# Kernel tuning notes

Measured on AMD Instinct MI355X. Metric: run time of the kernel, lower is better.

Reference implementation:

```python
import jax, jax.numpy as jnp
import numpy as np

N_NODES = 50000
N_EDGES = 800000
HID = 128
EDGE_FEAT = 4
NUM_G = 20
R_MIN, R_MAX = 0.0, 100.0  # r_max = 10.0**2


def _mlp2(x, w1, b1, w2, b2, act_last):
    y = jax.nn.relu(x @ w1 + b1)
    y = y @ w2 + b2
    return jax.nn.relu(y) if act_last else y


def _linear_init(key, fan_in, fan_out):
    kw, kb = jax.random.split(key)
    lim = 1.0 / np.sqrt(fan_in)
    w = jax.random.uniform(kw, (fan_in, fan_out), jnp.float32, -lim, lim)
    b = jax.random.uniform(kb, (fan_out,), jnp.float32, -lim, lim)
    return w, b


def setup_inputs():
    key = jax.random.key(0)
    ks = jax.random.split(key, 16)
    src = jax.random.randint(ks[0], (N_EDGES,), 0, N_NODES)
    dst = jax.random.randint(ks[1], (N_EDGES,), 0, N_NODES)
    edge_feat = jax.random.normal(ks[2], (N_EDGES, EDGE_FEAT), jnp.float32)
    h = jax.random.normal(ks[3], (N_NODES, HID), jnp.float32)
    x = jax.random.normal(ks[4], (N_NODES, 3), jnp.float32)
    ein = 2 * HID + EDGE_FEAT + NUM_G
    ew1, eb1 = _linear_init(ks[5], ein, HID)
    ew2, eb2 = _linear_init(ks[6], HID, HID)
    infw, infb = _linear_init(ks[7], HID, 1)
    xw1, xb1 = _linear_init(ks[8], HID, HID)
    xw2, xb2 = _linear_init(ks[9], HID, 1)
    nw1, nb1 = _linear_init(ks[10], 2 * HID, HID)
    nw2, nb2 = _linear_init(ks[11], HID, HID)
    return {"src": src, "dst": dst, "edge_feat": edge_feat, "h": h, "x": x,
            "ew1": ew1, "eb1": eb1, "ew2": ew2, "eb2": eb2,
            "infw": infw, "infb": infb,
            "xw1": xw1, "xb1": xb1, "xw2": xw2, "xb2": xb2,
            "nw1": nw1, "nb1": nb1, "nw2": nw2, "nb2": nb2}


def reference(src, dst, edge_feat, h, x,
              ew1, eb1, ew2, eb2, infw, infb,
              xw1, xb1, xw2, xb2, nw1, nb1, nw2, nb2):
    n_nodes = h.shape[0]
    rel_x = x[dst] - x[src]                      # [E, 3]
    r = jnp.sum(rel_x * rel_x, -1, keepdims=True)  # [E, 1]
    # GaussianSmearing expansion
    offsets = jnp.linspace(R_MIN, R_MAX, NUM_G)
    coeff = -0.5 / (offsets[1] - offsets[0]) ** 2
    r_feat = jnp.exp(coeff * (r - offsets) ** 2)  # [E, NUM_G]
    # edge message MLP (act_last=True)
    cat = jnp.concatenate([edge_feat, r_feat, h[dst], h[src]], axis=-1)
    mij = _mlp2(cat, ew1, eb1, ew2, eb2, act_last=True)  # [E, HID]
    eij = jax.nn.sigmoid(mij @ infw + infb)              # [E, 1]
    mi = jax.ops.segment_sum(mij * eij, dst, num_segments=n_nodes)  # [N, HID]
    h_new = h + _mlp2(jnp.concatenate([mi, h], -1), nw1, nb1, nw2, nb2, act_last=False)
    # coordinate update: (xi - xj) == rel_x
    x_scale = _mlp2(mij, xw1, xb1, xw2, xb2, act_last=False)  # [E, 1]
    delta_x = jax.ops.segment_sum(rel_x * x_scale, dst, num_segments=n_nodes)
    x_new = x + delta_x
    return h_new, x_new
```

## Files before the change

kernel.cpp:

```cpp
#include <hip/hip_runtime.h>

#define HID 128
#define NNODES 50000
#define NEDGES 800000

typedef __attribute__((ext_vector_type(8))) short short8;
typedef __attribute__((ext_vector_type(4))) float f32x4;

union U8 { short8 v; unsigned short u[8]; };

__device__ __forceinline__ unsigned short f2b(float f) {
  unsigned int u = __float_as_uint(f);
  u += 0x7FFFu + ((u >> 16) & 1u);
  return (unsigned short)(u >> 16);
}

__device__ __forceinline__ unsigned int pk2(float a, float b) {
  unsigned int ua = __float_as_uint(a);
  ua += 0x7FFFu + ((ua >> 16) & 1u);
  unsigned int ub = __float_as_uint(b);
  ub += 0x7FFFu + ((ub >> 16) & 1u);
  return (ua >> 16) | (ub & 0xFFFF0000u);
}

__device__ __forceinline__ unsigned int pk2h(float a, float b) {
  unsigned int ua = __float_as_uint(a) + 0x8000u;
  unsigned int ub = __float_as_uint(b) + 0x8000u;
  return (ua >> 16) | (ub & 0xFFFF0000u);
}

__device__ __forceinline__ void atomicPkAddBf16(unsigned short* addr, unsigned int packed) {
  asm volatile("global_atomic_pk_add_bf16 %0, %1, off" :: "v"(addr), "v"(packed) : "memory");
}

__device__ __forceinline__ int stage_chunk(int c0, int row) {
  return ((c0 >> 3) ^ (row & 7) ^ (((row >> 2) & 3) << 1)) & 15;
}

__global__ __launch_bounds__(256) void pack_kernel(
    const float* __restrict__ ew1, const float* __restrict__ ew2,
    const float* __restrict__ xw1, const float* __restrict__ nw1,
    const float* __restrict__ nw2, unsigned short* __restrict__ ws) {
  int i = blockIdx.x * 256 + threadIdx.x;
  const float* w; int base, ksrc;
  if (i < 36864)       { w = ew1; base = 0;      ksrc = 280; }
  else if (i < 53248)  { w = ew2; base = 36864;  ksrc = 128; }
  else if (i < 69632)  { w = xw1; base = 53248;  ksrc = 128; }
  else if (i < 102400) { w = nw1; base = 69632;  ksrc = 256; }
  else if (i < 118784) { w = nw2; base = 102400; ksrc = 128; }
  else return;
  int li = i - base;
  int j = li & 7, t = li >> 3;
  int col = t & 127, kg = t >> 7;
  int k = kg * 8 + j;
  float v = (k < ksrc) ? w[k * 128 + col] : 0.0f;
  ws[i] = f2b(v);
}

__global__ __launch_bounds__(256) void hpack_kernel(
    const float* __restrict__ h, unsigned short* __restrict__ hB) {
  int i = blockIdx.x * 256 + threadIdx.x;
  const float4* p = reinterpret_cast<const float4*>(h + (size_t)i * 8);
  float4 a = p[0], b = p[1];
  uint4 u;
  u.x = pk2(a.x, a.y); u.y = pk2(a.z, a.w);
  u.z = pk2(b.x, b.y); u.w = pk2(b.z, b.w);
  *reinterpret_cast<uint4*>(hB + (size_t)i * 8) = u;
}

template<int MODE>
__global__ __launch_bounds__(512, 8) void edge_kernel(
    const int* __restrict__ src, const int* __restrict__ dst,
    const float* __restrict__ ef, const float* __restrict__ h,
    const float* __restrict__ x,
    const float* __restrict__ eb1, const float* __restrict__ eb2,
    const float* __restrict__ infw, const float* __restrict__ infb,
    const float* __restrict__ xb1, const float* __restrict__ xw2,
    const float* __restrict__ xb2,
    const short8* __restrict__ W1p, const short8* __restrict__ W2p,
    const short8* __restrict__ XW1p,
    const unsigned short* __restrict__ hB,
    float* __restrict__ miF, unsigned short* __restrict__ miB,
    float* __restrict__ dx) {
  __shared__ __align__(16) char catB[64 * 576];
  __shared__ int dL[64], sL[64];
  __shared__ float relL[64][3];
  __shared__ float ppart[8][64];
  __shared__ float eijL[64];

  const int tid = threadIdx.x;
  const int e0 = blockIdx.x * 64;
  const int lane = tid & 63, w = tid >> 6;
  const int wm = w >> 2, wn = w & 3;
  const int lr = lane & 15, lg = lane >> 4;
  const int l7 = lr & 7, l3 = lr & 3;
  const int colb = wn*32 + lr;
  const int c00 = wn*32 + lg*4, c01 = c00 + 16;
  const int rbase = wm*32;

  {
    int row = tid >> 3, sub = tid & 7;
    int e = e0 + row;
    int s = src[e], d = dst[e];
    if (sub == 0) { sL[row] = s; dL[row] = d; }
    float rx = x[3*d+0] - x[3*s+0];
    float ry = x[3*d+1] - x[3*s+1];
    float rz = x[3*d+2] - x[3*s+2];
    if (sub == 1) { relL[row][0] = rx; relL[row][1] = ry; relL[row][2] = rz; }
    float r = rx*rx + ry*ry + rz*rz;
    const float step = 100.0f / 19.0f;
    const float co = -0.5f / (step * step);
    if (sub < 6) {
      float v4[4];
      if (sub == 0) {
        const float4 efv = reinterpret_cast<const float4*>(ef)[e];
        v4[0]=efv.x; v4[1]=efv.y; v4[2]=efv.z; v4[3]=efv.w;
      } else {
        #pragma unroll
        for (int q = 0; q < 4; ++q) {
          float g = (float)(sub*4 - 4 + q) * step;
          float t = r - g;
          v4[q] = __expf(co * t * t);
        }
      }
      int c = sub*4;
      int chunk = (c>>3) ^ (row&7);
      uint2 pv; pv.x = pk2h(v4[0], v4[1]); pv.y = pk2h(v4[2], v4[3]);
      *reinterpret_cast<uint2*>(catB + row*576 + (chunk<<4) + ((c&7)<<1)) = pv;
    } else if (sub == 6) {
      U8 z;
      #pragma unroll
      for (int j = 0; j < 8; ++j) z.u[j] = 0;
      *reinterpret_cast<short8*>(catB + row*576 + ((32 + (3 ^ (row&3)))<<4)) = z.v;
    }
  }

  #pragma unroll
  for (int it = 0; it < 4; ++it) {
    int i = tid + it*512;
    int row = i >> 5, c = i & 31;
    int node = (c < 16) ? dst[e0+row] : src[e0+row];
    int chunk = 3 + c;
    int sw = (chunk < 32) ? (chunk ^ (row&7)) : (32 + ((chunk&3) ^ (row&3)));
    if (MODE == 2) {
      short8 u = *reinterpret_cast<const short8*>(hB + (size_t)node*128 + (c&15)*8);
      *reinterpret_cast<short8*>(catB + row*576 + (sw<<4)) = u;
    } else {
      const float4* hp = reinterpret_cast<const float4*>(h + (size_t)node*128 + (c&15)*8);
      float4 a = hp[0], b = hp[1];
      uint4 u;
      u.x = pk2(a.x, a.y); u.y = pk2(a.z, a.w);
      u.z = pk2(b.x, b.y); u.w = pk2(b.z, b.w);
      *reinterpret_cast<uint4*>(catB + row*576 + (sw<<4)) = u;
    }
  }

  short8 p00 = W1p[(0*4+lg)*128 + colb], p01 = W1p[(0*4+lg)*128 + colb + 16];
  short8 p10 = W1p[(1*4+lg)*128 + colb], p11 = W1p[(1*4+lg)*128 + colb + 16];
  __syncthreads();

  f32x4 acc[2][2];
  #pragma unroll
  for (int t = 0; t < 2; ++t) { acc[t][0] = (f32x4)0.0f; acc[t][1] = (f32x4)0.0f; }
  #pragma unroll
  for (int kt = 0; kt < 9; ++kt) {
    int ch = (kt < 8) ? ((kt*4+lg) ^ l7) : (32 + (lg ^ l3));
    short8 a0 = *reinterpret_cast<const short8*>(catB + (rbase + 0*16 + lr)*576 + (ch<<4));
    short8 a1 = *reinterpret_cast<const short8*>(catB + (rbase + 1*16 + lr)*576 + (ch<<4));
    short8 b0, b1;
    if (kt == 0)      { b0 = p00; b1 = p01; }
    else if (kt == 1) { b0 = p10; b1 = p11; }
    else              { b0 = W1p[(kt*4+lg)*128 + colb]; b1 = W1p[(kt*4+lg)*128 + colb + 16]; }
    acc[0][0] = __builtin_amdgcn_mfma_f32_16x16x32_bf16(b0, a0, acc[0][0], 0, 0, 0);
    acc[0][1] = __builtin_amdgcn_mfma_f32_16x16x32_bf16(b1, a0, acc[0][1], 0, 0, 0);
    acc[1][0] = __builtin_amdgcn_mfma_f32_16x16x32_bf16(b0, a1, acc[1][0], 0, 0, 0);
    acc[1][1] = __builtin_amdgcn_mfma_f32_16x16x32_bf16(b1, a1, acc[1][1], 0, 0, 0);
  }
  __syncthreads();

  {
    float4 be0 = *reinterpret_cast<const float4*>(eb1 + c00);
    float4 be1 = *reinterpret_cast<const float4*>(eb1 + c01);
    #pragma unroll
    for (int t = 0; t < 2; ++t) {
      int row = rbase + t*16 + lr;
      char* rowB = catB + row*576;
      #pragma unroll
      for (int j = 0; j < 2; ++j) {
        const float4 be = j ? be1 : be0;
        int c0 = j ? c01 : c00;
        float v0 = fmaxf(acc[t][j][0] + be.x, 0.f);
        float v1 = fmaxf(acc[t][j][1] + be.y, 0.f);
        float v2 = fmaxf(acc[t][j][2] + be.z, 0.f);
        float v3 = fmaxf(acc[t][j][3] + be.w, 0.f);
        uint2 pv; pv.x = pk2h(v0, v1); pv.y = pk2h(v2, v3);
        int chunk = (c0>>3) ^ (row&7);
        *reinterpret_cast<uint2*>(rowB + (chunk<<4) + ((c0&7)<<1)) = pv;
      }
    }
  }
  __syncthreads();

  f32x4 acc2[2][2];
  #pragma unroll
  for (int t = 0; t < 2; ++t) { acc2[t][0] = (f32x4)0.0f; acc2[t][1] = (f32x4)0.0f; }
  #pragma unroll
  for (int kt = 0; kt < 4; ++kt) {
    int ch = (kt*4+lg) ^ l7;
    short8 a0 = *reinterpret_cast<const short8*>(catB + (rbase + 0*16 + lr)*576 + (ch<<4));
    short8 a1 = *reinterpret_cast<const short8*>(catB + (rbase + 1*16 + lr)*576 + (ch<<4));
    short8 b0 = W2p[(kt*4+lg)*128 + colb];
    short8 b1 = W2p[(kt*4+lg)*128 + colb + 16];
    acc2[0][0] = __builtin_amdgcn_mfma_f32_16x16x32_bf16(b0, a0, acc2[0][0], 0, 0, 0);
    acc2[0][1] = __builtin_amdgcn_mfma_f32_16x16x32_bf16(b1, a0, acc2[0][1], 0, 0, 0);
    acc2[1][0] = __builtin_amdgcn_mfma_f32_16x16x32_bf16(b0, a1, acc2[1][0], 0, 0, 0);
    acc2[1][1] = __builtin_amdgcn_mfma_f32_16x16x32_bf16(b1, a1, acc2[1][1], 0, 0, 0);
  }
  {
    float4 be0 = *reinterpret_cast<const float4*>(eb2 + c00);
    float4 be1 = *reinterpret_cast<const float4*>(eb2 + c01);
    float4 iw0 = *reinterpret_cast<const float4*>(infw + c00);
    float4 iw1 = *reinterpret_cast<const float4*>(infw + c01);
    float pl[2];
    #pragma unroll
    for (int t = 0; t < 2; ++t) {
      int row = rbase + t*16 + lr;
      char* rowB = catB + row*576;
      pl[t] = 0.f;
      #pragma unroll
      for (int j = 0; j < 2; ++j) {
        const float4 be = j ? be1 : be0;
        const float4 iw = j ? iw1 : iw0;
        int c0 = j ? c01 : c00;
        float v0 = fmaxf(acc2[t][j][0] + be.x, 0.f);
        float v1 = fmaxf(acc2[t][j][1] + be.y, 0.f);
        float v2 = fmaxf(acc2[t][j][2] + be.z, 0.f);
        float v3 = fmaxf(acc2[t][j][3] + be.w, 0.f);
        acc2[t][j][0]=v0; acc2[t][j][1]=v1; acc2[t][j][2]=v2; acc2[t][j][3]=v3;
        pl[t] += v0*iw.x + v1*iw.y + v2*iw.z + v3*iw.w;
        uint2 pv; pv.x = pk2h(v0, v1); pv.y = pk2h(v2, v3);
        int chunk = 16 + ((c0>>3) ^ (row&7));
        *reinterpret_cast<uint2*>(rowB + (chunk<<4) + ((c0&7)<<1)) = pv;
      }
    }
    #pragma unroll
    for (int t = 0; t < 2; ++t) {
      pl[t] += __shfl_xor(pl[t], 16, 64);
      pl[t] += __shfl_xor(pl[t], 32, 64);
    }
    if (lane < 16) {
      #pragma unroll
      for (int t = 0; t < 2; ++t) ppart[w][rbase + t*16 + lane] = pl[t];
    }
  }
  __syncthreads();

  if (tid < 64) {
    int wmr = tid >> 5;
    float s2 = infb[0] + ppart[wmr*4+0][tid] + ppart[wmr*4+1][tid]
                       + ppart[wmr*4+2][tid] + ppart[wmr*4+3][tid];
    eijL[tid] = 1.f / (1.f + __expf(-s2));
  }
  __syncthreads();

  if (MODE >= 1) {
    #pragma unroll
    for (int t = 0; t < 2; ++t) {
      int row = rbase + t*16 + lr;
      float e = eijL[row];
      char* rowB = catB + row*576;
      #pragma unroll
      for (int j = 0; j < 2; ++j) {
        int c0 = j ? c01 : c00;
        uint2 pv;
        pv.x = pk2h(acc2[t][j][0]*e, acc2[t][j][1]*e);
        pv.y = pk2h(acc2[t][j][2]*e, acc2[t][j][3]*e);
        *reinterpret_cast<uint2*>(rowB + (stage_chunk(c0, row)<<4) + ((c0&7)<<1)) = pv;
      }
    }
  } else {
    #pragma unroll
    for (int t = 0; t < 2; ++t) {
      int row = rbase + t*16 + lr;
      int d = dL[row];
      float e = eijL[row];
      float* fp = miF + (size_t)d*128;
      #pragma unroll
      for (int j = 0; j < 2; ++j) {
        int c0 = j ? c01 : c00;
        #pragma unroll
        for (int rg = 0; rg < 4; ++rg) atomicAdd(fp + c0 + rg, acc2[t][j][rg]*e);
      }
    }
  }
  __syncthreads();

  if (MODE >= 1) {
    int col0 = wn*32 + lr*2;
    #pragma unroll
    for (int t2 = 0; t2 < 8; ++t2) {
      int row = rbase + t2*4 + lg;
      int d = dL[row];
      unsigned int val = *reinterpret_cast<const unsigned int*>(
          catB + row*576 + (stage_chunk(col0, row)<<4) + ((col0&7)<<1));
      if (val) atomicPkAddBf16(miB + (size_t)d*128 + col0, val);
    }
  }

  f32x4 acc3[2][2];
  #pragma unroll
  for (int t = 0; t < 2; ++t) { acc3[t][0] = (f32x4)0.0f; acc3[t][1] = (f32x4)0.0f; }
  #pragma unroll
  for (int kt = 0; kt < 4; ++kt) {
    int ch = 16 + ((kt*4+lg) ^ l7);
    short8 a0 = *reinterpret_cast<const short8*>(catB + (rbase + 0*16 + lr)*576 + (ch<<4));
    short8 a1 = *reinterpret_cast<const short8*>(catB + (rbase + 1*16 + lr)*576 + (ch<<4));
    short8 b0 = XW1p[(kt*4+lg)*128 + colb];
    short8 b1 = XW1p[(kt*4+lg)*128 + colb + 16];
    acc3[0][0] = __builtin_amdgcn_mfma_f32_16x16x32_bf16(b0, a0, acc3[0][0], 0, 0, 0);
    acc3[0][1] = __builtin_amdgcn_mfma_f32_16x16x32_bf16(b1, a0, acc3[0][1], 0, 0, 0);
    acc3[1][0] = __builtin_amdgcn_mfma_f32_16x16x32_bf16(b0, a1, acc3[1][0], 0, 0, 0);
    acc3[1][1] = __builtin_amdgcn_mfma_f32_16x16x32_bf16(b1, a1, acc3[1][1], 0, 0, 0);
  }
  {
    float4 bx0 = *reinterpret_cast<const float4*>(xb1 + c00);
    float4 bx1 = *reinterpret_cast<const float4*>(xb1 + c01);
    float4 xw0 = *reinterpret_cast<const float4*>(xw2 + c00);
    float4 xw1v = *reinterpret_cast<const float4*>(xw2 + c01);
    float ql[2];
    #pragma unroll
    for (int t = 0; t < 2; ++t) {
      ql[t] = 0.f;
      #pragma unroll
      for (int j = 0; j < 2; ++j) {
        const float4 bx = j ? bx1 : bx0;
        const float4 xw = j ? xw1v : xw0;
        ql[t] += fmaxf(acc3[t][j][0] + bx.x, 0.f) * xw.x
               + fmaxf(acc3[t][j][1] + bx.y, 0.f) * xw.y
               + fmaxf(acc3[t][j][2] + bx.z, 0.f) * xw.z
               + fmaxf(acc3[t][j][3] + bx.w, 0.f) * xw.w;
      }
      ql[t] += __shfl_xor(ql[t], 16, 64);
      ql[t] += __shfl_xor(ql[t], 32, 64);
    }
    if (lane < 16) {
      #pragma unroll
      for (int t = 0; t < 2; ++t) ppart[w][rbase + t*16 + lane] = ql[t];
    }
  }
  __syncthreads();

  if (tid < 192) {
    int row = tid / 3, c = tid - row*3;
    int wmr = row >> 5;
    float q = xb2[0] + ppart[wmr*4+0][row] + ppart[wmr*4+1][row]
                     + ppart[wmr*4+2][row] + ppart[wmr*4+3][row];
    atomicAdd(dx + dL[row]*3 + c, relL[row][c] * q);
  }
}

template<int MODE>
__global__ __launch_bounds__(256) void node_kernel(
    const float* __restrict__ h, const float* __restrict__ x,
    const float* __restrict__ nb1, const float* __restrict__ nb2,
    const short8* __restrict__ NW1p, const short8* __restrict__ NW2p,
    const unsigned short* __restrict__ miB,
    const unsigned short* __restrict__ hB,
    float* __restrict__ out) {
  __shared__ __align__(16) char c2B[64 * 512];
  __shared__ __align__(16) char y3B[64 * 256];
  const int tid = threadIdx.x;
  const int n0 = blockIdx.x * 64;
  const float* mi = out;

  for (int i = tid; i < 64*32; i += 256) {
    int row = i >> 5, c = i & 31;
    int node = n0 + row;
    U8 u;
    if (node < NNODES) {
      if (c < 16 && MODE >= 1) {
        u.v = *reinterpret_cast<const short8*>(miB + (size_t)node*128 + c*8);
      } else if (c >= 16 && MODE == 2) {
        u.v = *reinterpret_cast<const short8*>(hB + (size_t)node*128 + (c-16)*8);
      } else {
        const float4* p = (c < 16)
          ? reinterpret_cast<const float4*>(mi + (size_t)node*128 + c*8)
          : reinterpret_cast<const float4*>(h + (size_t)node*128 + (c-16)*8);
        float4 a = p[0], b = p[1];
        uint4 uu;
        uu.x = pk2(a.x, a.y); uu.y = pk2(a.z, a.w);
        uu.z = pk2(b.x, b.y); uu.w = pk2(b.z, b.w);
        u.v = *reinterpret_cast<short8*>(&uu);
      }
    } else {
      #pragma unroll
      for (int j = 0; j < 8; ++j) u.u[j] = 0;
    }
    *reinterpret_cast<short8*>(c2B + row*512 + ((c ^ (row&7))<<4)) = u.v;
  }
  __syncthreads();

  const int lane = tid & 63, wave = tid >> 6;
  const int lr = lane & 15, lg = lane >> 4;
  const int rb = wave * 16;
  const int arow = rb + lr;

  f32x4 acc[8];
  #pragma unroll
  for (int nt = 0; nt < 8; ++nt) acc[nt] = (f32x4)0.0f;
  #pragma unroll
  for (int kt = 0; kt < 8; ++kt) {
    int chunk = kt*4 + lg;
    short8 a = *reinterpret_cast<const short8*>(c2B + arow*512 + ((chunk ^ (arow&7))<<4));
    const short8* bp = NW1p + chunk*128 + lr;
    #pragma unroll
    for (int nt = 0; nt < 8; ++nt)
      acc[nt] = __builtin_amdgcn_mfma_f32_16x16x32_bf16(a, bp[nt*16], acc[nt], 0, 0, 0);
  }
  #pragma unroll
  for (int nt = 0; nt < 8; ++nt) {
    int col = nt*16 + lr;
    float bias = nb1[col];
    #pragma unroll
    for (int r = 0; r < 4; ++r) {
      int row = rb + lg*4 + r;
      float v = fmaxf(acc[nt][r] + bias, 0.f);
      *reinterpret_cast<unsigned short*>(y3B + row*256 + (((col>>3) ^ (row&7))<<4) + ((col&7)<<1)) = f2b(v);
    }
  }

  f32x4 acc2[8];
  #pragma unroll
  for (int nt = 0; nt < 8; ++nt) acc2[nt] = (f32x4)0.0f;
  #pragma unroll
  for (int kt = 0; kt < 4; ++kt) {
    int chunk = kt*4 + lg;
    short8 a = *reinterpret_cast<const short8*>(y3B + arow*256 + ((chunk ^ (arow&7))<<4));
    const short8* bp = NW2p + chunk*128 + lr;
    #pragma unroll
    for (int nt = 0; nt < 8; ++nt)
      acc2[nt] = __builtin_amdgcn_mfma_f32_16x16x32_bf16(a, bp[nt*16], acc2[nt], 0, 0, 0);
  }
  __syncthreads();
  #pragma unroll
  for (int nt = 0; nt < 8; ++nt) {
    int col = nt*16 + lr;
    float b2 = nb2[col];
    #pragma unroll
    for (int r = 0; r < 4; ++r) {
      int row = rb + lg*4 + r;
      int node = n0 + row;
      if (node < NNODES) {
        int idx = node*128 + col;
        out[idx] = acc2[nt][r] + b2 + h[idx];
      }
    }
  }

  if (tid < 192) {
    int node = n0 + tid/3;
    if (node < NNODES) {
      int idx = node*3 + (tid%3);
      float* xo = out + NNODES*HID;
      xo[idx] = x[idx] + xo[idx];
    }
  }
}

extern "C" void kernel_launch(void* const* d_in, const int* in_sizes, int n_in,
                              void* d_out, int out_size, void* d_ws, size_t ws_size,
                              hipStream_t stream) {
  const int*   src  = (const int*)  d_in[0];
  const int*   dst  = (const int*)  d_in[1];
  const float* ef   = (const float*)d_in[2];
  const float* h    = (const float*)d_in[3];
  const float* x    = (const float*)d_in[4];
  const float* ew1  = (const float*)d_in[5];
  const float* eb1  = (const float*)d_in[6];
  const float* ew2  = (const float*)d_in[7];
  const float* eb2  = (const float*)d_in[8];
  const float* infw = (const float*)d_in[9];
  const float* infb = (const float*)d_in[10];
  const float* xw1  = (const float*)d_in[11];
  const float* xb1  = (const float*)d_in[12];
  const float* xw2  = (const float*)d_in[13];
  const float* xb2  = (const float*)d_in[14];
  const float* nw1  = (const float*)d_in[15];
  const float* nb1  = (const float*)d_in[16];
  const float* nw2  = (const float*)d_in[17];
  const float* nb2  = (const float*)d_in[18];

  float* out = (float*)d_out;
  float* miF = out;
  float* dxp = out + NNODES*HID;
  unsigned short* wsp = (unsigned short*)d_ws;
  unsigned short* miB = wsp + 118784;
  unsigned short* hBp = miB + (size_t)NNODES*HID;

  const size_t MIN = (size_t)NNODES*HID;
  size_t need1 = (118784u + MIN) * 2u;
  size_t need2 = (118784u + 2u*MIN) * 2u;
  int mode = (ws_size >= need2) ? 2 : (ws_size >= need1 ? 1 : 0);

  if (mode >= 1) {
    hipMemsetAsync(miB, 0, MIN*2, stream);
    hipMemsetAsync(dxp, 0, (size_t)NNODES*3*4, stream);
  } else {
    hipMemsetAsync(d_out, 0, (size_t)out_size * sizeof(float), stream);
  }

  pack_kernel<<<464, 256, 0, stream>>>(ew1, ew2, xw1, nw1, nw2, wsp);
  if (mode == 2) hpack_kernel<<<(NNODES*HID)/(256*8), 256, 0, stream>>>(h, hBp);

  if (mode == 2) {
    edge_kernel<2><<<NEDGES/64, 512, 0, stream>>>(
        src, dst, ef, h, x, eb1, eb2, infw, infb, xb1, xw2, xb2,
        (const short8*)wsp, (const short8*)(wsp + 36864), (const short8*)(wsp + 53248),
        hBp, miF, miB, dxp);
    node_kernel<2><<<(NNODES + 63)/64, 256, 0, stream>>>(
        h, x, nb1, nb2,
        (const short8*)(wsp + 69632), (const short8*)(wsp + 102400), miB, hBp, out);
  } else if (mode == 1) {
    edge_kernel<1><<<NEDGES/64, 512, 0, stream>>>(
        src, dst, ef, h, x, eb1, eb2, infw, infb, xb1, xw2, xb2,
        (const short8*)wsp, (const short8*)(wsp + 36864), (const short8*)(wsp + 53248),
        hBp, miF, miB, dxp);
    node_kernel<1><<<(NNODES + 63)/64, 256, 0, stream>>>(
        h, x, nb1, nb2,
        (const short8*)(wsp + 69632), (const short8*)(wsp + 102400), miB, hBp, out);
  } else {
    edge_kernel<0><<<NEDGES/64, 512, 0, stream>>>(
        src, dst, ef, h, x, eb1, eb2, infw, infb, xb1, xw2, xb2,
        (const short8*)wsp, (const short8*)(wsp + 36864), (const short8*)(wsp + 53248),
        hBp, miF, miB, dxp);
    node_kernel<0><<<(NNODES + 63)/64, 256, 0, stream>>>(
        h, x, nb1, nb2,
        (const short8*)(wsp + 69632), (const short8*)(wsp + 102400), miB, hBp, out);
  }
}
```

Before: 313.1 us.

## Sort edges by destination via counting sort before edge kernel

Adds a histogram, a single-block scan and a scatter kernel that build a permutation grouping edges by destination node. The edge kernel then processes edges in that order, so each block's atomic scatter-adds into the per-node accumulators hit nearby, mostly repeated addresses, which should reduce atomic contention and improve locality. In exchange it adds three extra launches, including a serial single-block scan over 50k counters, and an indirect load through the permutation. The edge order within a node is nondeterministic because it comes from atomics.

```diff
diff --git a/kernel.cpp b/kernel.cpp
--- a/kernel.cpp
+++ b/kernel.cpp
@@ -68,7 +68,46 @@
   *reinterpret_cast<uint4*>(hB + (size_t)i * 8) = u;
 }
 
-template<int MODE>
+__global__ __launch_bounds__(256) void hist_kernel(
+    const int* __restrict__ dst, int* __restrict__ cnt) {
+  int e = blockIdx.x * 256 + threadIdx.x;
+  if (e < NEDGES) atomicAdd(&cnt[dst[e]], 1);
+}
+
+__global__ __launch_bounds__(256) void scan_kernel(int* __restrict__ cnt) {
+  __shared__ int sums[256];
+  __shared__ int offs[256];
+  int t = threadIdx.x;
+  int base = t * 196;
+  int s = 0;
+  for (int i = 0; i < 196; ++i) {
+    int idx = base + i;
+    if (idx < NNODES) s += cnt[idx];
+  }
+  sums[t] = s;
+  __syncthreads();
+  if (t == 0) {
+    int r = 0;
+    for (int i = 0; i < 256; ++i) { offs[i] = r; r += sums[i]; }
+  }
+  __syncthreads();
+  int r = offs[t];
+  for (int i = 0; i < 196; ++i) {
+    int idx = base + i;
+    if (idx < NNODES) { int c = cnt[idx]; cnt[idx] = r; r += c; }
+  }
+}
+
+__global__ __launch_bounds__(256) void scatter_kernel(
+    const int* __restrict__ dst, int* __restrict__ start, int* __restrict__ perm) {
+  int e = blockIdx.x * 256 + threadIdx.x;
+  if (e < NEDGES) {
+    int p = atomicAdd(&start[dst[e]], 1);
+    perm[p] = e;
+  }
+}
+
+template<int MODE, int SORTED>
 __global__ __launch_bounds__(512, 8) void edge_kernel(
     const int* __restrict__ src, const int* __restrict__ dst,
     const float* __restrict__ ef, const float* __restrict__ h,
@@ -80,6 +119,7 @@
     const short8* __restrict__ W1p, const short8* __restrict__ W2p,
     const short8* __restrict__ XW1p,
     const unsigned short* __restrict__ hB,
+    const int* __restrict__ perm,
     float* __restrict__ miF, unsigned short* __restrict__ miB,
     float* __restrict__ dx) {
   __shared__ __align__(16) char catB[64 * 576];
@@ -100,7 +140,7 @@
 
   {
     int row = tid >> 3, sub = tid & 7;
-    int e = e0 + row;
+    int e = SORTED ? perm[e0 + row] : (e0 + row);
     int s = src[e], d = dst[e];
     if (sub == 0) { sL[row] = s; dL[row] = d; }
     float rx = x[3*d+0] - x[3*s+0];
@@ -139,7 +179,8 @@
   for (int it = 0; it < 4; ++it) {
     int i = tid + it*512;
     int row = i >> 5, c = i & 31;
-    int node = (c < 16) ? dst[e0+row] : src[e0+row];
+    int pe = SORTED ? perm[e0 + row] : (e0 + row);
+    int node = (c < 16) ? dst[pe] : src[pe];
     int chunk = 3 + c;
     int sw = (chunk < 32) ? (chunk ^ (row&7)) : (32 + ((chunk&3) ^ (row&3)));
     if (MODE == 2) {
@@ -496,11 +537,15 @@
   unsigned short* wsp = (unsigned short*)d_ws;
   unsigned short* miB = wsp + 118784;
   unsigned short* hBp = miB + (size_t)NNODES*HID;
+  int* cntp  = (int*)(wsp + 118784 + 2*(size_t)NNODES*HID);
+  int* permp = cntp + 50176;
 
   const size_t MIN = (size_t)NNODES*HID;
   size_t need1 = (118784u + MIN) * 2u;
   size_t need2 = (118784u + 2u*MIN) * 2u;
+  size_t need3 = need2 + (50176u + (size_t)NEDGES) * 4u;
   int mode = (ws_size >= need2) ? 2 : (ws_size >= need1 ? 1 : 0);
+  int sorted = (mode == 2 && ws_size >= need3) ? 1 : 0;
 
   if (mode >= 1) {
     hipMemsetAsync(miB, 0, MIN*2, stream);
@@ -512,27 +557,39 @@
   pack_kernel<<<464, 256, 0, stream>>>(ew1, ew2, xw1, nw1, nw2, wsp);
   if (mode == 2) hpack_kernel<<<(NNODES*HID)/(256*8), 256, 0, stream>>>(h, hBp);
 
-  if (mode == 2) {
-    edge_kernel<2><<<NEDGES/64, 512, 0, stream>>>(
+  if (sorted) {
+    hipMemsetAsync(cntp, 0, 50176*4, stream);
+    hist_kernel<<<(NEDGES+255)/256, 256, 0, stream>>>(dst, cntp);
+    scan_kernel<<<1, 256, 0, stream>>>(cntp);
+    scatter_kernel<<<(NEDGES+255)/256, 256, 0, stream>>>(dst, cntp, permp);
+    edge_kernel<2,1><<<NEDGES/64, 512, 0, stream>>>(
         src, dst, ef, h, x, eb1, eb2, infw, infb, xb1, xw2, xb2,
         (const short8*)wsp, (const short8*)(wsp + 36864), (const short8*)(wsp + 53248),
-        hBp, miF, miB, dxp);
+        hBp, permp, miF, miB, dxp);
+    node_kernel<2><<<(NNODES + 63)/64, 256, 0, stream>>>(
+        h, x, nb1, nb2,
+        (const short8*)(wsp + 69632), (const short8*)(wsp + 102400), miB, hBp, out);
+  } else if (mode == 2) {
+    edge_kernel<2,0><<<NEDGES/64, 512, 0, stream>>>(
+        src, dst, ef, h, x, eb1, eb2, infw, infb, xb1, xw2, xb2,
+        (const short8*)wsp, (const short8*)(wsp + 36864), (const short8*)(wsp + 53248),
+        hBp, permp, miF, miB, dxp);
     node_kernel<2><<<(NNODES + 63)/64, 256, 0, stream>>>(
         h, x, nb1, nb2,
         (const short8*)(wsp + 69632), (const short8*)(wsp + 102400), miB, hBp, out);
   } else if (mode == 1) {
-    edge_kernel<1><<<NEDGES/64, 512, 0, stream>>>(
+    edge_kernel<1,0><<<NEDGES/64, 512, 0, stream>>>(
         src, dst, ef, h, x, eb1, eb2, infw, infb, xb1, xw2, xb2,
         (const short8*)wsp, (const short8*)(wsp + 36864), (const short8*)(wsp + 53248),
-        hBp, miF, miB, dxp);
+        hBp, permp, miF, miB, dxp);
     node_kernel<1><<<(NNODES + 63)/64, 256, 0, stream>>>(
         h, x, nb1, nb2,
         (const short8*)(wsp + 69632), (const short8*)(wsp + 102400), miB, hBp, out);
   } else {
-    edge_kernel<0><<<NEDGES/64, 512, 0, stream>>>(
+    edge_kernel<0,0><<<NEDGES/64, 512, 0, stream>>>(
         src, dst, ef, h, x, eb1, eb2, infw, infb, xb1, xw2, xb2,
         (const short8*)wsp, (const short8*)(wsp + 36864), (const short8*)(wsp + 53248),
-        hBp, miF, miB, dxp);
+        hBp, permp, miF, miB, dxp);
     node_kernel<0><<<(NNODES + 63)/64, 256, 0, stream>>>(
         h, x, nb1, nb2,
         (const short8*)(wsp + 69632), (const short8*)(wsp + 102400), miB, hBp, out);
```

New measurement: 1.227 ms. 3.92x slower.
